# Performance work log

Hardware: AMD Instinct MI355X
Metric: run time of the kernel (lower is better)

Reference implementation:

```python
import jax, jax.numpy as jnp
import numpy as np

B, T, ENC, DEC, OUT = 256, 128, 256, 256, 3


def setup_inputs() -> dict:
    key = jax.random.key(0)
    ks = jax.random.split(key, 12)
    f32 = jnp.float32
    rn = lambda k, shape, s=0.1: (jax.random.normal(k, shape, dtype=f32) * s)
    return {
        "input_encoded": jax.random.normal(ks[0], (B, T, ENC), dtype=f32),
        "y_seq": jax.random.normal(ks[1], (B, T, OUT), dtype=f32),
        # attention linears
        "attn1_w": rn(ks[2], (ENC, 2 * DEC)), "attn1_b": jnp.zeros((ENC,), f32),
        "attn2_w": rn(ks[3], (ENC, ENC)), "attn2_b": jnp.zeros((ENC,), f32),
        "attn3_w": rn(ks[4], (1, ENC)), "attn3_b": jnp.zeros((1,), f32),
        # tilde: (ENC + 3) -> 2*DEC
        "tilde_w": rn(ks[5], (2 * DEC, ENC + OUT)), "tilde_b": jnp.zeros((2 * DEC,), f32),
        # single-layer LSTM, PyTorch gate order (i, f, g, o)
        "w_ih": rn(ks[6], (4 * DEC, 2 * DEC), 0.05), "w_hh": rn(ks[7], (4 * DEC, DEC), 0.05),
        "b_ih": jnp.zeros((4 * DEC,), f32), "b_hh": jnp.zeros((4 * DEC,), f32),
        # output head
        "fc1_w": rn(ks[8], (DEC, DEC + ENC)), "fc1_b": jnp.zeros((DEC,), f32),
        "fc2_w": rn(ks[9], (OUT, DEC)), "fc2_b": jnp.zeros((OUT,), f32),
    }


def _forward(input_encoded, y_seq, attn1_w, attn1_b, attn2_w, attn2_b,
             attn3_w, attn3_b, tilde_w, tilde_b, w_ih, w_hh, b_ih, b_hh,
             fc1_w, fc1_b, fc2_w, fc2_b):
    b, t_steps, enc = input_encoded.shape
    dec = w_hh.shape[1]
    # z2 = attn2(input_encoded) is loop-invariant: compute once. [B,T,ENC]
    z2 = jnp.einsum('bte,fe->btf', input_encoded, attn2_w) + attn2_b

    h0 = jnp.zeros((b, dec), input_encoded.dtype)
    c0 = jnp.zeros((b, dec), input_encoded.dtype)

    def step(carry, xs):
        h, c = carry
        t, y_t = xs  # y_t: [B,3]
        # attention over the T encoder positions conditioned on (h, c)
        hc = jnp.concatenate([h, c], axis=-1)                      # [B,2*DEC]
        z1 = hc @ attn1_w.T + attn1_b                              # [B,ENC]
        scores = jnp.einsum('btf,f->bt', jnp.tanh(z1[:, None, :] + z2), attn3_w[0]) + attn3_b[0]
        att = jax.nn.softmax(scores, axis=1)                       # [B,T]
        context = jnp.einsum('bt,bte->be', att, input_encoded)     # [B,ENC]
        # single LSTM step on tilde(y_t ++ context)
        y_tilde = jnp.concatenate([y_t, context], axis=-1) @ tilde_w.T + tilde_b
        gates = y_tilde @ w_ih.T + h @ w_hh.T + b_ih + b_hh        # [B,4*DEC]
        i_g, f_g, g_g, o_g = jnp.split(gates, 4, axis=-1)
        c_new = jax.nn.sigmoid(f_g) * c + jax.nn.sigmoid(i_g) * jnp.tanh(g_g)
        h_new = jax.nn.sigmoid(o_g) * jnp.tanh(c_new)
        # original skips the state update on the last timestep
        upd = t < t_steps - 1
        h2 = jnp.where(upd, h_new, h)
        c2 = jnp.where(upd, c_new, c)
        return (h2, c2), jnp.concatenate([h2, context], axis=-1)   # [B,DEC+ENC]

    xs = (jnp.arange(t_steps), jnp.transpose(y_seq, (1, 0, 2)))
    (_, _), th = jax.lax.scan(step, (h0, c0), xs)
    total_hidden = jnp.transpose(th, (1, 0, 2))                    # [B,T,DEC+ENC]
    # incre=True branch: fc2(fc1(total_hidden))
    return (total_hidden @ fc1_w.T + fc1_b) @ fc2_w.T + fc2_b      # [B,T,OUT]


def reference(input_encoded, y_seq, attn1_w, attn1_b, attn2_w, attn2_b,
              attn3_w, attn3_b, tilde_w, tilde_b, w_ih, w_hh, b_ih, b_hh,
              fc1_w, fc1_b, fc2_w, fc2_b):
    return _forward(input_encoded, y_seq, attn1_w, attn1_b, attn2_w, attn2_b,
                    attn3_w, attn3_b, tilde_w, tilde_b, w_ih, w_hh, b_ih, b_hh,
                    fc1_w, fc1_b, fc2_w, fc2_b)
```

## Files before the change

### kernel.cpp

```cpp
#include <hip/hip_runtime.h>


#define TT 128
#define SCL 2.885390081777927f

typedef _Float16 h2v __attribute__((ext_vector_type(2)));
typedef _Float16 f16x4 __attribute__((ext_vector_type(4)));
typedef _Float16 f16x8 __attribute__((ext_vector_type(8)));

__device__ __forceinline__ float fdot2(h2v a, h2v b, float c) {
#if __has_builtin(__builtin_amdgcn_fdot2)
  return __builtin_amdgcn_fdot2(a, b, c, false);
#else
  return c + (float)a[0] * (float)b[0] + (float)a[1] * (float)b[1];
#endif
}

__device__ __forceinline__ float exp2_fast(float x) {
#if __has_builtin(__builtin_amdgcn_exp2f)
  return __builtin_amdgcn_exp2f(x);
#else
  return exp2f(x);
#endif
}
__device__ __forceinline__ float rcp_fast(float x) {
#if __has_builtin(__builtin_amdgcn_rcpf)
  return __builtin_amdgcn_rcpf(x);
#else
  return 1.f / x;
#endif
}

__device__ __forceinline__ float tanh_scaled(float s) {
  return fmaf(-2.f, rcp_fast(exp2_fast(s) + 1.f), 1.f);
}
__device__ __forceinline__ float fast_sig(float x) {
  return rcp_fast(1.f + __expf(-x));
}
__device__ __forceinline__ float fast_tanh(float x) {
  return tanh_scaled(x * SCL);
}

__device__ __forceinline__ float dot8(f16x8 w, f16x8 h, float acc) {
  h2v w0 = __builtin_shufflevector(w, w, 0, 1), h0 = __builtin_shufflevector(h, h, 0, 1);
  h2v w1 = __builtin_shufflevector(w, w, 2, 3), h1 = __builtin_shufflevector(h, h, 2, 3);
  h2v w2 = __builtin_shufflevector(w, w, 4, 5), h2 = __builtin_shufflevector(h, h, 4, 5);
  h2v w3 = __builtin_shufflevector(w, w, 6, 7), h3 = __builtin_shufflevector(h, h, 6, 7);
  acc = fdot2(w0, h0, acc);
  acc = fdot2(w1, h1, acc);
  acc = fdot2(w2, h2, acc);
  acc = fdot2(w3, h3, acc);
  return acc;
}


__global__ void k_transpose(const float* __restrict__ src, float* __restrict__ dst,
                            int R, int C) {
  int idx = blockIdx.x * 256 + threadIdx.x;
  if (idx >= R * C) return;
  int r = idx / C, c = idx - r * C;
  dst[(size_t)c * R + r] = src[idx];
}

__global__ __launch_bounds__(256) void k_z2x(const float* __restrict__ x,
                                             const float* __restrict__ a2wT,
                                             const float* __restrict__ a2b,
                                             const float* __restrict__ a1b,
                                             _Float16* __restrict__ z2h,
                                             _Float16* __restrict__ xTg) {
  __shared__ float xt[16][257];
  const int r0 = blockIdx.x * 16;
  const int tid = threadIdx.x;
  for (int idx = tid; idx < 16 * 256; idx += 256) {
    int rr = idx >> 8, e = idx & 255;
    xt[rr][e] = x[(size_t)(r0 + rr) * 256 + e];
  }
  __syncthreads();
  const int f = tid;
  float bias = a2b[f] + a1b[f];
  float acc[16];
#pragma unroll
  for (int rr = 0; rr < 16; ++rr) acc[rr] = bias;
  for (int e = 0; e < 256; ++e) {
    float w = a2wT[(size_t)e * 256 + f];
#pragma unroll
    for (int rr = 0; rr < 16; ++rr) acc[rr] += w * xt[rr][e];
  }
#pragma unroll
  for (int rr = 0; rr < 16; ++rr)
    z2h[(size_t)(r0 + rr) * 256 + f] = (_Float16)(acc[rr] * SCL);
  const int bb = r0 >> 7, t0 = r0 & 127;
  f16x8 lo, hi;
#pragma unroll
  for (int rr = 0; rr < 8; ++rr) lo[rr] = (_Float16)xt[rr][f];
#pragma unroll
  for (int rr = 0; rr < 8; ++rr) hi[rr] = (_Float16)xt[8 + rr][f];
  _Float16* d = &xTg[((size_t)bb * 256 + f) * 128 + t0];
  *(f16x8*)d = lo;
  *(f16x8*)(d + 8) = hi;
}

__global__ void k_pack_a1(const float* __restrict__ a1w, _Float16* __restrict__ dst) {
  int idx = blockIdx.x * 256 + threadIdx.x;
  int j = idx & 7, f = (idx >> 3) & 255, kc = idx >> 11;
  dst[idx] = (_Float16)(a1w[(size_t)f * 512 + kc * 8 + j] * SCL);
}

__global__ void k_pack_whh(const float* __restrict__ whh, _Float16* __restrict__ dst) {
  int idx = blockIdx.x * 256 + threadIdx.x;
  int j = idx & 7, n = (idx >> 3) & 1023, kc = idx >> 13;
  dst[idx] = (_Float16)whh[(size_t)n * 256 + kc * 8 + j];
}

__global__ __launch_bounds__(320) void k_wcomb(const float* __restrict__ w_ih,
                                               const float* __restrict__ tilde_w,
                                               const float* __restrict__ tilde_b,
                                               const float* __restrict__ b_ih,
                                               const float* __restrict__ b_hh,
                                               _Float16* __restrict__ wc8,
                                               float* __restrict__ bcomb) {
  __shared__ float wrow[512];
  __shared__ float bred[320];
  const int n = blockIdx.x;
  const int tid = threadIdx.x;
  for (int j = tid; j < 512; j += 320) wrow[j] = w_ih[(size_t)n * 512 + j];
  __syncthreads();
  if (tid < 264) {
    float acc = 0.f;
    if (tid < 259)
      for (int j = 0; j < 512; ++j) acc += wrow[j] * tilde_w[(size_t)j * 259 + tid];
    wc8[(size_t)(tid >> 3) * 8192 + n * 8 + (tid & 7)] = (_Float16)acc;
  }
  float p = 0.f;
  for (int j = tid; j < 512; j += 320) p += wrow[j] * tilde_b[j];
  bred[tid] = p;
  __syncthreads();
  if (tid == 0) {
    float s = 0.f;
    for (int j = 0; j < 320; ++j) s += bred[j];
    bcomb[n] = s + b_ih[n] + b_hh[n];
  }
}

__global__ __launch_bounds__(512) void k_whead(const float* __restrict__ fc1_w,
                                               const float* __restrict__ fc1_b,
                                               const float* __restrict__ fc2_w,
                                               const float* __restrict__ fc2_b,
                                               float* __restrict__ whead,
                                               float* __restrict__ bhead) {
  const int k = threadIdx.x;
#pragma unroll
  for (int o = 0; o < 3; ++o) {
    float acc = 0.f;
    for (int j = 0; j < 256; ++j) acc += fc2_w[o * 256 + j] * fc1_w[(size_t)j * 512 + k];
    whead[o * 512 + k] = acc;
  }
  if (k < 3) {
    float acc = fc2_b[k];
    for (int j = 0; j < 256; ++j) acc += fc2_w[k * 256 + j] * fc1_b[j];
    bhead[k] = acc;
  }
}


__global__ __launch_bounds__(1024, 4) void k_decoder(
    const _Float16* __restrict__ z2g,
    const _Float16* __restrict__ xTg,
    const float* __restrict__ yg,
    const float* __restrict__ a3w,
    const _Float16* __restrict__ a1p8,
    const _Float16* __restrict__ whh8,
    const _Float16* __restrict__ wc8,
    const float* __restrict__ bcomb,
    const float* __restrict__ whead,
    const float* __restrict__ bhead,
    float* __restrict__ outg)
{
  __shared__ __align__(16) _Float16 z2s[128][260];
  __shared__ __align__(16) _Float16 xs[256][132];
  __shared__ float zpart[1024];
  __shared__ float scpart[1024];
  __shared__ float cpart[1024];
  __shared__ float gbuf[1024];
  __shared__ float z1c[256];
  __shared__ float hbuf[256], cbuf[256], ctxs[256], w3s[256];
  __shared__ __align__(16) _Float16 hc8[512];
  __shared__ __align__(16) _Float16 u8[264];
  __shared__ float attv[128];
  __shared__ float sred[8];

  const int b = blockIdx.x;
  const int tid = threadIdx.x;

  {
    const f16x8* zsrc = (const f16x8*)(z2g + (size_t)b * TT * 256);
    for (int c = tid; c < 4096; c += 1024) {
      int t = c >> 5, fc = c & 31;
      f16x8 v = zsrc[c];
      f16x4 lo = __builtin_shufflevector(v, v, 0, 1, 2, 3);
      f16x4 hi = __builtin_shufflevector(v, v, 4, 5, 6, 7);
      _Float16* d = &z2s[t][fc * 8];
      *(f16x4*)d = lo;
      *(f16x4*)(d + 4) = hi;
    }
    const f16x8* xsrc = (const f16x8*)(xTg + (size_t)b * 256 * 128);
    for (int c = tid; c < 4096; c += 1024) {
      int e = c >> 4, tc = c & 15;
      f16x8 v = xsrc[c];
      f16x4 lo = __builtin_shufflevector(v, v, 0, 1, 2, 3);
      f16x4 hi = __builtin_shufflevector(v, v, 4, 5, 6, 7);
      _Float16* d = &xs[e][tc * 8];
      *(f16x4*)d = lo;
      *(f16x4*)(d + 4) = hi;
    }
  }
  if (tid < 256) {
    w3s[tid] = a3w[tid];
    hbuf[tid] = 0.f; cbuf[tid] = 0.f;
    hc8[tid] = (_Float16)0.f; hc8[256 + tid] = (_Float16)0.f;
  }
  if (tid >= 259 && tid < 264) u8[tid] = (_Float16)0.f;
  __syncthreads();

  const int f_z = tid & 255;
  const int qz = tid >> 8;
  const _Float16* pa = a1p8 + ((size_t)(qz * 16) * 256 + f_z) * 8;
  const _Float16* pw = whh8 + (size_t)tid * 8;
  const _Float16* pc = wc8 + (size_t)tid * 8;
  const float bc = bcomb[tid];

  float whr[8], bh = 0.f;
  if (tid < 192) {
    int o = tid >> 6, lane = tid & 63;
#pragma unroll
    for (int q2 = 0; q2 < 8; ++q2) whr[q2] = whead[o * 512 + lane + (q2 << 6)];
    bh = bhead[o];
  }

  for (int t = 0; t < TT; ++t) {
    float yreg = (tid < 3) ? yg[(size_t)(b * TT + t) * 3 + tid] : 0.f;

    float ghr;
    {
      float za0 = 0.f, za1 = 0.f;
#pragma unroll 4
      for (int i = 0; i < 16; i += 2) {
        f16x8 w0 = *(const f16x8*)(pa + (size_t)i * 2048);
        f16x8 w1 = *(const f16x8*)(pa + (size_t)(i + 1) * 2048);
        f16x8 h0 = *(const f16x8*)&hc8[(qz * 16 + i) * 8];
        f16x8 h1 = *(const f16x8*)&hc8[(qz * 16 + i + 1) * 8];
        za0 = dot8(w0, h0, za0);
        za1 = dot8(w1, h1, za1);
      }
      zpart[tid] = za0 + za1;
      float g0 = 0.f, g1 = 0.f;
#pragma unroll 4
      for (int kc = 0; kc < 32; kc += 2) {
        f16x8 w0 = *(const f16x8*)(pw + (size_t)kc * 8192);
        f16x8 w1 = *(const f16x8*)(pw + (size_t)(kc + 1) * 8192);
        f16x8 h0 = *(const f16x8*)&hc8[kc * 8];
        f16x8 h1 = *(const f16x8*)&hc8[(kc + 1) * 8];
        g0 = dot8(w0, h0, g0);
        g1 = dot8(w1, h1, g1);
      }
      ghr = g0 + g1;
    }
    __syncthreads();

    if (tid < 256)
      z1c[tid] = zpart[tid] + zpart[tid + 256] + zpart[tid + 512] + zpart[tid + 768];
    __syncthreads();

    {
      int tp = tid & 127, q = tid >> 7, f0 = q * 32;
      const _Float16* zr = &z2s[tp][f0];
      float acc = 0.f;
#pragma unroll
      for (int i = 0; i < 8; ++i) {
        f16x4 zz = *(const f16x4*)(zr + i * 4);
#pragma unroll
        for (int j = 0; j < 4; ++j) {
          int f = f0 + i * 4 + j;
          acc = fmaf(tanh_scaled(z1c[f] + (float)zz[j]), w3s[f], acc);
        }
      }
      scpart[tid] = acc;
    }
    __syncthreads();

    if (tid < 128) {
      float sc = scpart[tid] + scpart[tid + 128] + scpart[tid + 256] + scpart[tid + 384] +
                 scpart[tid + 512] + scpart[tid + 640] + scpart[tid + 768] + scpart[tid + 896];
      float e = __expf(sc);
      attv[tid] = e;
      float s = e;
#pragma unroll
      for (int off = 32; off > 0; off >>= 1) s += __shfl_xor(s, off);
      if ((tid & 63) == 0) sred[2 + (tid >> 6)] = s;
    }
    __syncthreads();

    {
      int e = tid & 255, th4 = tid >> 8;
      const _Float16* xr = &xs[e][th4 * 32];
      float acc = 0.f;
#pragma unroll
      for (int i = 0; i < 8; ++i) {
        f16x4 xv = *(const f16x4*)(xr + i * 4);
#pragma unroll
        for (int j = 0; j < 4; ++j)
          acc = fmaf(attv[th4 * 32 + i * 4 + j], (float)xv[j], acc);
      }
      cpart[tid] = acc;
    }
    __syncthreads();

    const float rsum = rcp_fast(sred[2] + sred[3]);
    if (tid < 256) {
      float cv = (cpart[tid] + cpart[tid + 256] + cpart[tid + 512] + cpart[tid + 768]) * rsum;
      ctxs[tid] = cv;
      u8[3 + tid] = (_Float16)cv;
    }
    if (tid < 3) u8[tid] = (_Float16)yreg;
    __syncthreads();

    {
      float a0 = 0.f, a1 = 0.f;
#pragma unroll 4
      for (int kc = 0; kc < 32; kc += 2) {
        f16x8 w0 = *(const f16x8*)(pc + (size_t)kc * 8192);
        f16x8 w1 = *(const f16x8*)(pc + (size_t)(kc + 1) * 8192);
        f16x8 u0 = *(const f16x8*)&u8[kc * 8];
        f16x8 u1 = *(const f16x8*)&u8[(kc + 1) * 8];
        a0 = dot8(w0, u0, a0);
        a1 = dot8(w1, u1, a1);
      }
      a0 = dot8(*(const f16x8*)(pc + (size_t)32 * 8192), *(const f16x8*)&u8[256], a0);
      gbuf[tid] = a0 + a1 + ghr + bc;
    }
    __syncthreads();

    if (tid < 256) {
      float gi = gbuf[tid], gf = gbuf[tid + 256], gg = gbuf[tid + 512], go = gbuf[tid + 768];
      float cn = fast_sig(gf) * cbuf[tid] + fast_sig(gi) * fast_tanh(gg);
      float hn = fast_sig(go) * fast_tanh(cn);
      if (t < TT - 1) {
        hbuf[tid] = hn; cbuf[tid] = cn;
        hc8[tid] = (_Float16)hn; hc8[256 + tid] = (_Float16)cn;
      }
    }
    __syncthreads();

    if (tid < 192) {
      int o = tid >> 6, lane = tid & 63;
      float acc = 0.f;
#pragma unroll
      for (int q2 = 0; q2 < 8; ++q2) {
        int k = lane + (q2 << 6);
        float v = (k < 256) ? hbuf[k] : ctxs[k - 256];
        acc = fmaf(whr[q2], v, acc);
      }
#pragma unroll
      for (int off = 32; off > 0; off >>= 1) acc += __shfl_xor(acc, off);
      if (lane == 0) outg[(size_t)(b * TT + t) * 3 + o] = acc + bh;
    }
  }
}


extern "C" void kernel_launch(void* const* d_in, const int* in_sizes, int n_in,
                              void* d_out, int out_size, void* d_ws, size_t ws_size,
                              hipStream_t stream) {
  const float* x   = (const float*)d_in[0];
  const float* y   = (const float*)d_in[1];
  const float* a1w = (const float*)d_in[2];
  const float* a1b = (const float*)d_in[3];
  const float* a2w = (const float*)d_in[4];
  const float* a2b = (const float*)d_in[5];
  const float* a3w = (const float*)d_in[6];
  const float* tw  = (const float*)d_in[8];
  const float* tb  = (const float*)d_in[9];
  const float* wih = (const float*)d_in[10];
  const float* whh = (const float*)d_in[11];
  const float* bih = (const float*)d_in[12];
  const float* bhh = (const float*)d_in[13];
  const float* f1w = (const float*)d_in[14];
  const float* f1b = (const float*)d_in[15];
  const float* f2w = (const float*)d_in[16];
  const float* f2b = (const float*)d_in[17];
  float* out = (float*)d_out;

  float* ws = (float*)d_ws;
  _Float16* z2h  = (_Float16*)ws;
  _Float16* xT   = (_Float16*)(ws + 4194304);
  float* a2wT    = ws + 8388608;
  _Float16* a1p8 = (_Float16*)(ws + 8388608 + 65536);
  _Float16* whh8 = (_Float16*)(ws + 8388608 + 131072);
  _Float16* wc8  = (_Float16*)(ws + 8388608 + 262144);
  float* bcomb   = ws + 8388608 + 262144 + 135168;
  float* whead   = bcomb + 1024;
  float* bhead   = whead + 1536;

  k_transpose<<<dim3((256 * 256 + 255) / 256), dim3(256), 0, stream>>>(a2w, a2wT, 256, 256);
  k_z2x<<<dim3(2048), dim3(256), 0, stream>>>(x, a2wT, a2b, a1b, z2h, xT);
  k_pack_a1<<<dim3(512), dim3(256), 0, stream>>>(a1w, a1p8);
  k_pack_whh<<<dim3(1024), dim3(256), 0, stream>>>(whh, whh8);
  k_wcomb<<<dim3(1024), dim3(320), 0, stream>>>(wih, tw, tb, bih, bhh, wc8, bcomb);
  k_whead<<<dim3(1), dim3(512), 0, stream>>>(f1w, f1b, f2w, f2b, whead, bhead);

  k_decoder<<<dim3(256), dim3(1024), 0, stream>>>(z2h, xT, y, a3w, a1p8, whh8, wc8,
                                                  bcomb, whead, bhead, out);
}
```

Before: 1.884 ms.

## Replace shared-memory partial reductions with warp shuffles and drop barriers

Remaps thread-to-work assignment in the attention z1, score and context phases so the split-K partials sit in adjacent lanes and are summed with shuffle-xor instead of shared arrays. This removes three __syncthreads per timestep and the zpart/scpart/cpart buffers. The softmax exp and sum are fused into the score phase, and every thread now sums 16 wave partials itself. Padded indexing (stride 33) avoids LDS bank conflicts, at the cost of more shuffle instructions and changed global access patterns for the attn1 weights.

```diff
diff --git a/kernel.cpp b/kernel.cpp
--- a/kernel.cpp
+++ b/kernel.cpp
@@ -178,16 +178,14 @@
 {
   __shared__ __align__(16) _Float16 z2s[128][260];
   __shared__ __align__(16) _Float16 xs[256][132];
-  __shared__ float zpart[1024];
-  __shared__ float scpart[1024];
-  __shared__ float cpart[1024];
   __shared__ float gbuf[1024];
-  __shared__ float z1c[256];
-  __shared__ float hbuf[256], cbuf[256], ctxs[256], w3s[256];
+  __shared__ float z1c[264];
+  __shared__ float w3p[264];
+  __shared__ float attv[132];
+  __shared__ float hbuf[256], cbuf[256], ctxs[256];
   __shared__ __align__(16) _Float16 hc8[512];
   __shared__ __align__(16) _Float16 u8[264];
-  __shared__ float attv[128];
-  __shared__ float sred[8];
+  __shared__ float sred[16];
 
   const int b = blockIdx.x;
   const int tid = threadIdx.x;
@@ -215,18 +213,19 @@
     }
   }
   if (tid < 256) {
-    w3s[tid] = a3w[tid];
+    w3p[tid + (tid >> 5)] = a3w[tid];
     hbuf[tid] = 0.f; cbuf[tid] = 0.f;
     hc8[tid] = (_Float16)0.f; hc8[256 + tid] = (_Float16)0.f;
   }
   if (tid >= 259 && tid < 264) u8[tid] = (_Float16)0.f;
   __syncthreads();
 
-  const int f_z = tid & 255;
-  const int qz = tid >> 8;
-  const _Float16* pa = a1p8 + ((size_t)(qz * 16) * 256 + f_z) * 8;
+  const int f_z = tid >> 2;
+  const int kq = tid & 3;
+  const f16x8* pa = (const f16x8*)a1p8 + ((size_t)(kq * 16) * 256 + f_z);
   const _Float16* pw = whh8 + (size_t)tid * 8;
   const _Float16* pc = wc8 + (size_t)tid * 8;
+  const f16x8* hcv = (const f16x8*)hc8;
   const float bc = bcomb[tid];
 
   float whr[8], bh = 0.f;
@@ -245,21 +244,25 @@
       float za0 = 0.f, za1 = 0.f;
 #pragma unroll 4
       for (int i = 0; i < 16; i += 2) {
-        f16x8 w0 = *(const f16x8*)(pa + (size_t)i * 2048);
-        f16x8 w1 = *(const f16x8*)(pa + (size_t)(i + 1) * 2048);
-        f16x8 h0 = *(const f16x8*)&hc8[(qz * 16 + i) * 8];
-        f16x8 h1 = *(const f16x8*)&hc8[(qz * 16 + i + 1) * 8];
+        f16x8 w0 = pa[(size_t)i * 256];
+        f16x8 w1 = pa[(size_t)(i + 1) * 256];
+        f16x8 h0 = hcv[kq * 16 + i];
+        f16x8 h1 = hcv[kq * 16 + i + 1];
         za0 = dot8(w0, h0, za0);
         za1 = dot8(w1, h1, za1);
       }
-      zpart[tid] = za0 + za1;
+      float za = za0 + za1;
+      za += __shfl_xor(za, 1);
+      za += __shfl_xor(za, 2);
+      if (kq == 0) z1c[f_z + (f_z >> 5)] = za;
+
       float g0 = 0.f, g1 = 0.f;
 #pragma unroll 4
       for (int kc = 0; kc < 32; kc += 2) {
         f16x8 w0 = *(const f16x8*)(pw + (size_t)kc * 8192);
         f16x8 w1 = *(const f16x8*)(pw + (size_t)(kc + 1) * 8192);
-        f16x8 h0 = *(const f16x8*)&hc8[kc * 8];
-        f16x8 h1 = *(const f16x8*)&hc8[(kc + 1) * 8];
+        f16x8 h0 = hcv[kc];
+        f16x8 h1 = hcv[kc + 1];
         g0 = dot8(w0, h0, g0);
         g1 = dot8(w1, h1, g1);
       }
@@ -267,41 +270,38 @@
     }
     __syncthreads();
 
-    if (tid < 256)
-      z1c[tid] = zpart[tid] + zpart[tid + 256] + zpart[tid + 512] + zpart[tid + 768];
-    __syncthreads();
-
     {
-      int tp = tid & 127, q = tid >> 7, f0 = q * 32;
-      const _Float16* zr = &z2s[tp][f0];
+      int tp = tid >> 3, q = tid & 7;
+      const _Float16* zr = &z2s[tp][q * 32];
       float acc = 0.f;
 #pragma unroll
       for (int i = 0; i < 8; ++i) {
         f16x4 zz = *(const f16x4*)(zr + i * 4);
 #pragma unroll
         for (int j = 0; j < 4; ++j) {
-          int f = f0 + i * 4 + j;
-          acc = fmaf(tanh_scaled(z1c[f] + (float)zz[j]), w3s[f], acc);
+          int jj = i * 4 + j;
+          acc = fmaf(tanh_scaled(z1c[q * 33 + jj] + (float)zz[j]), w3p[q * 33 + jj], acc);
         }
       }
-      scpart[tid] = acc;
+      acc += __shfl_xor(acc, 1);
+      acc += __shfl_xor(acc, 2);
+      acc += __shfl_xor(acc, 4);
+      float e = __expf(acc);
+      if (q == 0) attv[tp + (tp >> 5)] = e;
+      float v = (q == 0) ? e : 0.f;
+      v += __shfl_xor(v, 8);
+      v += __shfl_xor(v, 16);
+      v += __shfl_xor(v, 32);
+      if ((tid & 63) == 0) sred[tid >> 6] = v;
     }
     __syncthreads();
 
-    if (tid < 128) {
-      float sc = scpart[tid] + scpart[tid + 128] + scpart[tid + 256] + scpart[tid + 384] +
-                 scpart[tid + 512] + scpart[tid + 640] + scpart[tid + 768] + scpart[tid + 896];
-      float e = __expf(sc);
-      attv[tid] = e;
-      float s = e;
-#pragma unroll
-      for (int off = 32; off > 0; off >>= 1) s += __shfl_xor(s, off);
-      if ((tid & 63) == 0) sred[2 + (tid >> 6)] = s;
-    }
-    __syncthreads();
-
     {
-      int e = tid & 255, th4 = tid >> 8;
+      float ssum = 0.f;
+#pragma unroll
+      for (int w = 0; w < 16; ++w) ssum += sred[w];
+      const float rsum = rcp_fast(ssum);
+      int e = tid >> 2, th4 = tid & 3;
       const _Float16* xr = &xs[e][th4 * 32];
       float acc = 0.f;
 #pragma unroll
@@ -309,19 +309,17 @@
         f16x4 xv = *(const f16x4*)(xr + i * 4);
 #pragma unroll
         for (int j = 0; j < 4; ++j)
-          acc = fmaf(attv[th4 * 32 + i * 4 + j], (float)xv[j], acc);
-      }
-      cpart[tid] = acc;
-    }
-    __syncthreads();
-
-    const float rsum = rcp_fast(sred[2] + sred[3]);
-    if (tid < 256) {
-      float cv = (cpart[tid] + cpart[tid + 256] + cpart[tid + 512] + cpart[tid + 768]) * rsum;
-      ctxs[tid] = cv;
-      u8[3 + tid] = (_Float16)cv;
-    }
-    if (tid < 3) u8[tid] = (_Float16)yreg;
+          acc = fmaf(attv[th4 * 33 + i * 4 + j], (float)xv[j], acc);
+      }
+      acc += __shfl_xor(acc, 1);
+      acc += __shfl_xor(acc, 2);
+      if (th4 == 0) {
+        float cv = acc * rsum;
+        ctxs[e] = cv;
+        u8[3 + e] = (_Float16)cv;
+      }
+      if (tid < 3) u8[tid] = (_Float16)yreg;
+    }
     __syncthreads();
 
     {
```

After: 2.595 ms. +37.7%, slower.
